# Kernel tuning notes

Hardware: AMD Instinct MI355X
Metric: run time of the kernel (lower is better)

Reference implementation:

```python
import jax, jax.numpy as jnp
import numpy as np

DIM = 64   # model dim == d_inner (expand=1)
Hh = 64
Ww = 64
BATCH = 4
D_IN = 64
N_ST = 8   # d_state
DT_R = 4   # dt_rank = ceil(dim/16)
K = 4      # depthwise conv kernel
NB = 8     # total CrossMambaBlocks: 4 (depth=1) + 4 final cross blocks


def setup_inputs():
    key = jax.random.key(0)
    ks = iter(jax.random.split(key, 40))
    def rn(shape, s=0.02):
        return jax.random.normal(next(ks), shape, jnp.float32) * s
    A_init = jnp.log(jnp.tile(jnp.arange(1, N_ST + 1, dtype=jnp.float32), (NB, D_IN, 1)))
    return dict(
        img1=rn((BATCH, DIM, Hh, Ww), 1.0), img2=rn((BATCH, DIM, Hh, Ww), 1.0),
        img1_sum=rn((BATCH, DIM, Hh, Ww), 1.0), img2_sum=rn((BATCH, DIM, Hh, Ww), 1.0),
        norm0_w=jnp.ones((NB, DIM)), norm0_b=jnp.zeros((NB, DIM)),
        norm1_w=jnp.ones((NB, DIM)), norm1_b=jnp.zeros((NB, DIM)),
        in_w=rn((NB, 2 * D_IN, DIM)), in_b=jnp.zeros((NB, 2 * D_IN)),
        conv_w_f=rn((NB, D_IN, 1, K), 0.1), conv_b_f=jnp.zeros((NB, D_IN)),
        conv_w_b=rn((NB, D_IN, 1, K), 0.1), conv_b_b=jnp.zeros((NB, D_IN)),
        xproj_w_f=rn((NB, DT_R + 2 * N_ST, D_IN)), xproj_w_b=rn((NB, DT_R + 2 * N_ST, D_IN)),
        dtproj_w_f=rn((NB, D_IN, DT_R), 0.1), dtproj_b_f=jnp.zeros((NB, D_IN)),
        dtproj_w_b=rn((NB, D_IN, DT_R), 0.1), dtproj_b_b=jnp.zeros((NB, D_IN)),
        A_log_f=A_init, A_log_b=A_init,
        D_f=jnp.ones((NB, D_IN)), D_b=jnp.ones((NB, D_IN)),
        ln_w=jnp.ones((NB, D_IN)), ln_b=jnp.zeros((NB, D_IN)),
        mout_w=rn((NB, DIM, D_IN)), mout_b=jnp.zeros((NB, DIM)),
        fop_w=rn((DIM, 2 * DIM)), fop_b=jnp.zeros((DIM,)),
    )


def _ln(x, w, b):
    m = x.mean(-1, keepdims=True)
    v = ((x - m) ** 2).mean(-1, keepdims=True)
    return (x - m) * jax.lax.rsqrt(v + 1e-5) * w + b


def _dwconv(x, w, b):
    # x: [b,L,d], w: [d,1,K] depthwise causal conv along L
    y = jax.lax.conv_general_dilated(
        x.transpose(0, 2, 1), w, (1,), [(K - 1, 0)],
        dimension_numbers=('NCH', 'OIH', 'NCH'),
        feature_group_count=x.shape[-1])
    return y.transpose(0, 2, 1) + b


def _ssm(u, dt, Bm, Cm, A, Dm):
    # u,dt: [b,L,d]; Bm,Cm: [b,L,n]; A: [d,n]; Dm: [d]
    dA = jnp.exp(dt[..., None] * A)                 # [b,L,d,n]
    dBu = (dt * u)[..., None] * Bm[:, :, None, :]   # [b,L,d,n]
    def step(h, xs):
        dA_t, dBu_t, C_t = xs
        h = dA_t * h + dBu_t
        return h, jnp.einsum('bdn,bn->bd', h, C_t)
    h0 = jnp.zeros(u.shape[:1] + A.shape, u.dtype)
    _, ys = jax.lax.scan(step, h0, (jnp.moveaxis(dA, 1, 0), jnp.moveaxis(dBu, 1, 0), jnp.moveaxis(Cm, 1, 0)))
    return jnp.moveaxis(ys, 0, 1) + u * Dm


def _direction(x_in, extra, conv_w, conv_b, xproj_w, dtproj_w, dtproj_b, A_log, Dm, flip):
    if flip:
        x_in = x_in[:, ::-1]
        extra = extra[:, ::-1]
    u = jax.nn.silu(_dwconv(x_in, conv_w, conv_b))
    dbl = jnp.einsum('bld,ed->ble', extra, xproj_w)     # cross: dt/B/C from extra embedding
    dtr = dbl[..., :DT_R]
    Bm = dbl[..., DT_R:DT_R + N_ST]
    Cm = dbl[..., DT_R + N_ST:]
    dt = jax.nn.softplus(jnp.einsum('blr,dr->bld', dtr, dtproj_w) + dtproj_b)
    y = _ssm(u, dt, Bm, Cm, -jnp.exp(A_log), Dm)
    if flip:
        y = y[:, ::-1]
    return y


def _cross_block(i, x, extra, p):
    skip = x
    x = _ln(x, p['norm0_w'][i], p['norm0_b'][i])
    extra = _ln(extra, p['norm1_w'][i], p['norm1_b'][i])
    xz = jnp.einsum('bld,ed->ble', x, p['in_w'][i]) + p['in_b'][i]
    x_in, z = xz[..., :D_IN], xz[..., D_IN:]
    y_f = _direction(x_in, extra, p['conv_w_f'][i], p['conv_b_f'][i], p['xproj_w_f'][i],
                     p['dtproj_w_f'][i], p['dtproj_b_f'][i], p['A_log_f'][i], p['D_f'][i], False)
    y_b = _direction(x_in, extra, p['conv_w_b'][i], p['conv_b_b'][i], p['xproj_w_b'][i],
                     p['dtproj_w_b'][i], p['dtproj_b_b'][i], p['A_log_b'][i], p['D_b'][i], True)
    y = 0.5 * (y_f + y_b)                    # if_devide_out=True
    y = _ln(y, p['ln_w'][i], p['ln_b'][i])   # use_norm=True
    y = y * jax.nn.silu(z)
    out = jnp.einsum('bld,ed->ble', y, p['mout_w'][i]) + p['mout_b'][i]
    return out + skip


def _forward(img1, img2, img1_sum, img2_sum, norm0_w, norm0_b, norm1_w, norm1_b, in_w, in_b,
             conv_w_f, conv_b_f, conv_w_b, conv_b_b, xproj_w_f, xproj_w_b,
             dtproj_w_f, dtproj_b_f, dtproj_w_b, dtproj_b_b, A_log_f, A_log_b,
             D_f, D_b, ln_w, ln_b, mout_w, mout_b, fop_w, fop_b):
    p = dict(norm0_w=norm0_w, norm0_b=norm0_b, norm1_w=norm1_w, norm1_b=norm1_b,
             in_w=in_w, in_b=in_b, conv_w_f=conv_w_f, conv_b_f=conv_b_f,
             conv_w_b=conv_w_b, conv_b_b=conv_b_b, xproj_w_f=xproj_w_f, xproj_w_b=xproj_w_b,
             dtproj_w_f=dtproj_w_f, dtproj_b_f=dtproj_b_f, dtproj_w_b=dtproj_w_b,
             dtproj_b_b=dtproj_b_b, A_log_f=A_log_f, A_log_b=A_log_b, D_f=D_f, D_b=D_b,
             ln_w=ln_w, ln_b=ln_b, mout_w=mout_w, mout_b=mout_b)
    def seq(t):
        b, c, h, w = t.shape
        return t.reshape(b, c, h * w).transpose(0, 2, 1)   # b (h w) c
    s1, s2, s1s, s2s = seq(img1), seq(img2), seq(img1_sum), seq(img2_sum)
    # depth=1 cross-fusion loop
    s1 = _cross_block(0, s1, s1s, p)
    s2 = _cross_block(1, s2, s2s, p)
    s1s = _cross_block(2, s1s, s1, p)
    s2s = _cross_block(3, s2s, s2, p)
    # final cross blocks
    i1l = _cross_block(4, s1, s2, p)
    i1g = _cross_block(5, s1, s2s, p)
    i2l = _cross_block(6, s2, s1, p)
    i2g = _cross_block(7, s2, s1s, p)
    c1 = jnp.concatenate([i1l, i1g], -1)
    c2 = jnp.concatenate([i2l, i2g], -1)
    fusion = jnp.einsum('ble,ce->blc', 0.5 * (c1 + c2), fop_w) + fop_b
    b = img1.shape[0]
    return fusion.transpose(0, 2, 1).reshape(b, DIM, Hh, Ww)


def reference(img1, img2, img1_sum, img2_sum, norm0_w, norm0_b, norm1_w, norm1_b, in_w, in_b,
              conv_w_f, conv_b_f, conv_w_b, conv_b_b, xproj_w_f, xproj_w_b,
              dtproj_w_f, dtproj_b_f, dtproj_w_b, dtproj_b_b, A_log_f, A_log_b,
              D_f, D_b, ln_w, ln_b, mout_w, mout_b, fop_w, fop_b):
    return _forward(img1, img2, img1_sum, img2_sum, norm0_w, norm0_b, norm1_w, norm1_b, in_w, in_b,
                    conv_w_f, conv_b_f, conv_w_b, conv_b_b, xproj_w_f, xproj_w_b,
                    dtproj_w_f, dtproj_b_f, dtproj_w_b, dtproj_b_b, A_log_f, A_log_b,
                    D_f, D_b, ln_w, ln_b, mout_w, mout_b, fop_w, fop_b)
```

## Files before the change

### kernel.cpp

```cpp
#include <hip/hip_runtime.h>
#include <hip/hip_bf16.h>

#define BX 4
#define LX 4096
#define DX 64
#define NX 8
#define TCH 16
#define NCH 256
#define BLD (BX*LX*DX)

typedef unsigned short u16;
typedef __attribute__((ext_vector_type(8))) short v8s;
typedef __attribute__((ext_vector_type(4))) float v4f;

#define L2E 1.44269504088896f
#define LN2 0.69314718055994531f

__device__ __forceinline__ float b2f(u16 u){ return __uint_as_float(((unsigned)u)<<16); }
__device__ __forceinline__ u16 f2b(float f){
  unsigned u = __float_as_uint(f);
  unsigned r = (u + 0x7FFFu + ((u>>16)&1u)) >> 16;
  return (u16)r;
}
__device__ __forceinline__ float siluf(float x){
  return x * __builtin_amdgcn_rcpf(1.f + __builtin_amdgcn_exp2f(-x*L2E));
}
__device__ __forceinline__ float softplusf(float x){
  const float t = __builtin_amdgcn_exp2f(-fabsf(x)*L2E);
  return fmaxf(x, 0.f) + LN2 * __builtin_amdgcn_logf(1.f + t);
}

__device__ __forceinline__ v4f mfma16(v8s a, v8s b, v4f c){
  return __builtin_amdgcn_mfma_f32_16x16x32_bf16(a, b, c, 0, 0, 0);
}
__device__ __forceinline__ void split8(const float* v, v8s& hi, v8s& lo){
  #pragma unroll
  for(int j=0;j<8;j++){
    const short h = (short)f2b(v[j]);
    hi[j] = h;
    lo[j] = (short)f2b(v[j] - b2f((u16)h));
  }
}
__device__ __forceinline__ void afrag(const float* tile, int lane, int k0, v8s& hi, v8s& lo){
  const float* p = tile + (lane&15)*72 + k0 + ((lane>>4)<<3);
  float v[8];
  const float4 a = *(const float4*)(p);
  const float4 b = *(const float4*)(p+4);
  v[0]=a.x; v[1]=a.y; v[2]=a.z; v[3]=a.w;
  v[4]=b.x; v[5]=b.y; v[6]=b.z; v[7]=b.w;
  split8(v, hi, lo);
}

struct Ctx {
  const float *nw0,*nb0,*nw1,*nb1;
  const float *inw,*inb;
  const float *convw,*convb;
  const float *xproj;
  const float *dtw,*dtb;
  const float *A2,*Dp;
  const float *lnw,*lnb;
  const float *moutw,*moutb;
  const float *fopw,*fopb;
  const u16 *wih,*wil,*wxh,*wxl,*wmh,*wml,*wfh,*wfl;
  float *act[4], *outc[4];
  float *xin[4], *zz[4], *dbl[4], *yy[4], *Pp[4], *qq[4], *hin[4];
};

struct BlkDesc { int i; const float* x; const float* e; float* out; int slot; };
struct StageArgs { BlkDesc d[4]; };

struct PrepEnt { const void* src; float* dst; int n; int mode; };
struct PrepAll { PrepEnt a[26]; };

__global__ __launch_bounds__(256) void k_prep(PrepAll pa, const u16* df){
  const bool isbf = (df[0] == 0x3F80u);
  PrepEnt p = pa.a[blockIdx.y];
  int idx = blockIdx.x*256 + threadIdx.x;
  if(idx < p.n){
    float v = isbf ? b2f(((const u16*)p.src)[idx]) : ((const float*)p.src)[idx];
    if(p.mode==2) v = -__expf(v) * L2E;
    p.dst[idx] = v;
  }
}

struct WPrep { const float* src; u16* dh; u16* dl; int E; int KS; int kind; int i; };
struct WPrepAll { WPrep a[25]; };

__global__ __launch_bounds__(64) void k_prepw(WPrepAll wa, const float* xprojbase){
  WPrep p = wa.a[blockIdx.y];
  const int NT = (p.E + 15) >> 4;
  const int idx = blockIdx.x;
  if(idx >= NT*p.KS) return;
  const int ct = idx / p.KS, ks = idx % p.KS;
  const int lane = threadIdx.x;
  const int g  = ct*16 + (lane & 15);
  const int k0 = ks*32 + ((lane>>4)<<3);
  const int K  = p.KS*32;
  bool valid; const float* srcp = nullptr;
  if(p.kind == 1){
    valid = (g < 40);
    if(valid){ const int dir = g/20, e = g - dir*20;
      srcp = xprojbase + ((size_t)(dir*8 + p.i)*20 + e)*64 + k0; }
  } else {
    valid = (g < p.E);
    if(valid) srcp = p.src + (size_t)g*K + k0;
  }
  float v[8];
  #pragma unroll
  for(int j=0;j<8;j++) v[j] = valid ? srcp[j] : 0.f;
  v8s hi, lo; split8(v, hi, lo);
  const size_t o = ((size_t)idx*64 + lane)*8;
  *(v8s*)(p.dh + o) = hi;
  *(v8s*)(p.dl + o) = lo;
}

struct SeqArgs { const void* src[4]; };

__global__ __launch_bounds__(256) void k_seq(SeqArgs s, Ctx c, const u16* df){
  const bool isbf = (df[0] == 0x3F80u);
  __shared__ float ld[64*65];
  const int t = blockIdx.z, b = blockIdx.y, l0 = blockIdx.x*64;
  float* dst = c.act[t];
  const int tx = threadIdx.x, ty = threadIdx.y;
  if(isbf){
    const u16* src = (const u16*)s.src[t];
    #pragma unroll
    for(int k=0;k<16;k++){ int d = k*4+ty; ld[d*65+tx] = b2f(src[(size_t)(b*64+d)*LX + l0+tx]); }
  } else {
    const float* src = (const float*)s.src[t];
    #pragma unroll
    for(int k=0;k<16;k++){ int d = k*4+ty; ld[d*65+tx] = src[(size_t)(b*64+d)*LX + l0+tx]; }
  }
  __syncthreads();
  #pragma unroll
  for(int k=0;k<16;k++){ int p = k*4+ty; dst[(size_t)(b*LX + l0+p)*64 + tx] = ld[tx*65+p]; }
}

__device__ __forceinline__ void coop72(float* sb, const float* g, int t){
  #pragma unroll
  for(int k=0;k<4;k++){
    const int idx = k*256 + t;
    const int row = idx >> 4;
    const int c4  = (idx & 15) << 2;
    *(float4*)(sb + row*72 + c4) = *(const float4*)(g + (size_t)row*64 + c4);
  }
}
__device__ __forceinline__ void coop72_avg(float* sb, const float* g0, const float* g1, int t){
  #pragma unroll
  for(int k=0;k<4;k++){
    const int idx = k*256 + t;
    const int row = idx >> 4;
    const int c4  = (idx & 15) << 2;
    const float4 a = *(const float4*)(g0 + (size_t)row*64 + c4);
    const float4 b = *(const float4*)(g1 + (size_t)row*64 + c4);
    float4 o; o.x=0.5f*(a.x+b.x); o.y=0.5f*(a.y+b.y); o.z=0.5f*(a.z+b.z); o.w=0.5f*(a.w+b.w);
    *(float4*)(sb + row*72 + c4) = o;
  }
}

__device__ __forceinline__ void ln72(float* sb, int lane, const float* w, const float* b){
  float r[64];
  float* p = sb + lane*72;
  #pragma unroll
  for(int cc=0;cc<64;cc+=4){ float4 v = *(const float4*)(p+cc); r[cc]=v.x; r[cc+1]=v.y; r[cc+2]=v.z; r[cc+3]=v.w; }
  float m=0.f;
  #pragma unroll
  for(int d=0;d<64;d++) m += r[d];
  m *= (1.f/64.f);
  float va=0.f;
  #pragma unroll
  for(int d=0;d<64;d++){ float t=r[d]-m; va += t*t; }
  va *= (1.f/64.f);
  const float rs = rsqrtf(va + 1e-5f);
  #pragma unroll
  for(int d=0;d<64;d++) r[d] = (r[d]-m)*rs*w[d] + b[d];
  #pragma unroll
  for(int cc=0;cc<64;cc+=4){ float4 v={r[cc],r[cc+1],r[cc+2],r[cc+3]}; *(float4*)(p+cc)=v; }
}

__global__ __launch_bounds__(256) void k_front(Ctx c, StageArgs sa){
  __shared__ __align__(16) float sx[64*72];
  __shared__ __align__(16) float se[64*72];
  const BlkDesc bd = sa.d[blockIdx.y];
  const int i = bd.i;
  const int tile = blockIdx.x;
  const int b = tile >> 6;
  const int l0 = (tile & 63) << 6;
  const int bl0 = b*LX + l0;
  const int t = threadIdx.x;
  const int wave = t >> 6, lane = t & 63;

  coop72(sx, bd.x + (size_t)bl0*64, t);
  coop72(se, bd.e + (size_t)bl0*64, t);
  __syncthreads();
  if(wave == 0)      ln72(sx, lane, c.nw0 + i*64, c.nb0 + i*64);
  else if(wave == 1) ln72(se, lane, c.nw1 + i*64, c.nb1 + i*64);
  __syncthreads();

  const int m0 = wave*16;
  const int q  = lane >> 4;
  const int n15 = lane & 15;

  {
    v8s ah[2], al[2];
    afrag(sx + m0*72, lane, 0,  ah[0], al[0]);
    afrag(sx + m0*72, lane, 32, ah[1], al[1]);
    const v8s* WH = (const v8s*)c.wih + (size_t)i*1024;
    const v8s* WL = (const v8s*)c.wil + (size_t)i*1024;
    #pragma unroll 1
    for(int ct=0; ct<8; ct++){
      const int colg = ct*16 + n15;
      const float bias = c.inb[i*128 + colg];
      v4f acc = {bias, bias, bias, bias};
      #pragma unroll
      for(int ks=0; ks<2; ks++){
        const v8s wh = WH[(ct*2+ks)*64 + lane];
        const v8s wl = WL[(ct*2+ks)*64 + lane];
        acc = mfma16(ah[ks], wl, acc);
        acc = mfma16(al[ks], wh, acc);
        acc = mfma16(ah[ks], wh, acc);
      }
      float* baseo = (colg < 64) ? c.xin[bd.slot] : c.zz[bd.slot];
      const int col = colg & 63;
      #pragma unroll
      for(int r=0;r<4;r++){
        const int row = m0 + q*4 + r;
        baseo[(size_t)(bl0+row)*64 + col] = acc[r];
      }
    }
  }
  {
    v8s ah[2], al[2];
    afrag(se + m0*72, lane, 0,  ah[0], al[0]);
    afrag(se + m0*72, lane, 32, ah[1], al[1]);
    const v8s* WH = (const v8s*)c.wxh + (size_t)i*384;
    const v8s* WL = (const v8s*)c.wxl + (size_t)i*384;
    #pragma unroll 1
    for(int ct=0; ct<3; ct++){
      v4f acc = {0.f,0.f,0.f,0.f};
      #pragma unroll
      for(int ks=0; ks<2; ks++){
        const v8s wh = WH[(ct*2+ks)*64 + lane];
        const v8s wl = WL[(ct*2+ks)*64 + lane];
        acc = mfma16(ah[ks], wl, acc);
        acc = mfma16(al[ks], wh, acc);
        acc = mfma16(ah[ks], wh, acc);
      }
      const int g = ct*16 + n15;
      if(g < 40){
        const int dir = (g >= 20);
        const int e = g - dir*20;
        float* dp = c.dbl[bd.slot] + (size_t)dir*((size_t)BX*LX*20);
        #pragma unroll
        for(int r=0;r<4;r++){
          const int row = m0 + q*4 + r;
          dp[(size_t)(bl0+row)*20 + e] = acc[r];
        }
      }
    }
  }
}

template<int PASS>
__device__ __forceinline__ void scan_body(const Ctx& c, const StageArgs& sa){
  __shared__ float meta[TCH*20];
  const int zid = blockIdx.z;
  const int j = zid >> 1, dir = zid & 1;
  const BlkDesc bd = sa.d[j];
  const int i = bd.i, slot = bd.slot;
  const int ch = blockIdx.x, b = blockIdx.y;
  const int d = threadIdx.x;
  const int pb = (dir*8 + i)*64 + d;

  const float4 cwv = *(const float4*)(c.convw + (size_t)pb*4);
  const float  cbv = c.convb[pb];
  const float4 dwv = *(const float4*)(c.dtw + (size_t)pb*4);
  const float  dtbv = c.dtb[pb];
  const float4 A2a = *(const float4*)(c.A2 + (size_t)pb*8);
  const float4 A2b = *(const float4*)(c.A2 + (size_t)pb*8 + 4);
  float A2[8] = {A2a.x,A2a.y,A2a.z,A2a.w,A2b.x,A2b.y,A2b.z,A2b.w};

  {
    const float4* s = (const float4*)(c.dbl[slot] + (size_t)dir*((size_t)BX*LX*20)
                                      + (size_t)(b*LX + ch*TCH)*20);
    float4* dst = (float4*)meta;
    #pragma unroll
    for(int k=0;k<2;k++){ int idx = k*64 + d; if(idx < 80) dst[idx] = s[idx]; }
  }
  __syncthreads();

  const float* X = c.xin[slot] + (size_t)b*LX*64 + d;
  float h[8];
  if(PASS==1){
    #pragma unroll
    for(int n=0;n<8;n++) h[n]=0.f;
  } else {
    const float* hp = c.hin[slot] + (size_t)(dir*NCH + ch)*((size_t)BX*512) + (size_t)b*512 + d;
    #pragma unroll
    for(int n=0;n<8;n++) h[n] = hp[n*64];
  }
  const float Dv = (PASS==3) ? c.Dp[pb] : 0.f;
  float* Y = (PASS==3) ? (c.yy[slot] + (size_t)(dir*BX + b)*LX*64 + d) : (float*)0;

  int lbase, sgn;
  if(dir==0){ lbase = ch*TCH;          sgn =  1; }
  else      { lbase = ch*TCH + TCH-1;  sgn = -1; }
  float w0,w1,w2;
  { int p0 = lbase - 3*sgn; w0 = (p0>=0 && p0<LX)? X[(size_t)p0*64] : 0.f; }
  { int p1 = lbase - 2*sgn; w1 = (p1>=0 && p1<LX)? X[(size_t)p1*64] : 0.f; }
  { int p2 = lbase - 1*sgn; w2 = (p2>=0 && p2<LX)? X[(size_t)p2*64] : 0.f; }

  const float* Xp = X + (size_t)lbase*64;
  float* Yp = (PASS==3) ? (Y + (size_t)lbase*64) : (float*)0;
  const float* mp = meta + (dir ? (TCH-1)*20 : 0);
  const int xstep = sgn*64;
  const int mstep = sgn*20;

  float S = 0.f;
  #pragma unroll 4
  for(int t=0;t<TCH;t++){
    const float xc = *Xp;
    const float u = siluf(cwv.x*w0 + cwv.y*w1 + cwv.z*w2 + cwv.w*xc + cbv);
    const float4 m0  = *(const float4*)(mp);
    const float4 mb0 = *(const float4*)(mp+4);
    const float4 mb1 = *(const float4*)(mp+8);
    const float dt = softplusf(m0.x*dwv.x + m0.y*dwv.y + m0.z*dwv.z + m0.w*dwv.w + dtbv);
    const float du = dt*u;
    const float Bv[8] = {mb0.x,mb0.y,mb0.z,mb0.w,mb1.x,mb1.y,mb1.z,mb1.w};
    #pragma unroll
    for(int n=0;n<8;n++){
      const float dA = __builtin_amdgcn_exp2f(dt*A2[n]);
      h[n] = dA*h[n] + du*Bv[n];
    }
    if(PASS==3){
      const float4 mc0 = *(const float4*)(mp+12);
      const float4 mc1 = *(const float4*)(mp+16);
      const float Cv[8] = {mc0.x,mc0.y,mc0.z,mc0.w,mc1.x,mc1.y,mc1.z,mc1.w};
      float yv = u*Dv;
      #pragma unroll
      for(int n=0;n<8;n++) yv += h[n]*Cv[n];
      *Yp = yv;
      Yp += xstep;
    } else {
      S += dt;
    }
    w0=w1; w1=w2; w2=xc;
    Xp += xstep; mp += mstep;
  }
  if(PASS==1){
    float* Pw = c.Pp[slot] + (size_t)(dir*NCH + ch)*((size_t)BX*512) + (size_t)b*512 + d;
    float* Qw = c.qq[slot] + (size_t)(dir*NCH + ch)*((size_t)BX*512) + (size_t)b*512 + d;
    #pragma unroll
    for(int n=0;n<8;n++){
      Pw[n*64] = __builtin_amdgcn_exp2f(A2[n]*S);
      Qw[n*64] = h[n];
    }
  }
}

__global__ __launch_bounds__(64) void k_scan1(Ctx c, StageArgs sa){ scan_body<1>(c, sa); }
__global__ __launch_bounds__(64) void k_scan3(Ctx c, StageArgs sa){ scan_body<3>(c, sa); }

__global__ __launch_bounds__(64) void k_mid(Ctx c, StageArgs sa){
  const int b = blockIdx.x >> 3;
  const int seg = blockIdx.x & 7;
  const int dir = blockIdx.y & 1, j = blockIdx.y >> 1;
  const BlkDesc bd = sa.d[j];
  const int slot = bd.slot;
  const int nd = seg*64 + threadIdx.x;
  const size_t base = (size_t)dir*NCH*((size_t)BX*512) + (size_t)b*512 + nd;
  const size_t STR = (size_t)BX*512;
  const float* P = c.Pp[slot] + base;
  const float* Q = c.qq[slot] + base;
  float* H = c.hin[slot] + base;
  float h = 0.f;
  float Pv[16], Qv[16];
  #pragma unroll 1
  for(int g=0; g<NCH/16; g++){
    #pragma unroll
    for(int k=0;k<16;k++){
      const int ch = dir ? (NCH-1 - (g*16+k)) : (g*16+k);
      Pv[k] = P[(size_t)ch*STR]; Qv[k] = Q[(size_t)ch*STR];
    }
    #pragma unroll
    for(int k=0;k<16;k++){
      const int ch = dir ? (NCH-1 - (g*16+k)) : (g*16+k);
      H[(size_t)ch*STR] = h;
      h = fmaf(Pv[k], h, Qv[k]);
    }
  }
}

__global__ __launch_bounds__(256) void k_back(Ctx c, StageArgs sa){
  __shared__ __align__(16) float sy[64*72];
  __shared__ __align__(16) float sz[64*72];
  __shared__ __align__(16) float sk[64*72];
  const BlkDesc bd = sa.d[blockIdx.y];
  const int i = bd.i, slot = bd.slot;
  const int tile = blockIdx.x;
  const int b = tile >> 6;
  const int l0 = (tile & 63) << 6;
  const int bl0 = b*LX + l0;
  const int t = threadIdx.x;
  const int wave = t >> 6, lane = t & 63;

  coop72_avg(sy, c.yy[slot] + (size_t)b*LX*64 + (size_t)l0*64,
                 c.yy[slot] + (size_t)(BX+b)*LX*64 + (size_t)l0*64, t);
  coop72(sz, c.zz[slot] + (size_t)bl0*64, t);
  coop72(sk, bd.x + (size_t)bl0*64, t);
  __syncthreads();
  if(wave == 0){
    ln72(sy, lane, c.lnw + i*64, c.lnb + i*64);
    float* p = sy + lane*72;
    const float* zp = sz + lane*72;
    #pragma unroll
    for(int d=0;d<64;d++){ const float zv = zp[d]; p[d] *= siluf(zv)/(zv==0.f?1.f:zv)*zv; }
  }
  __syncthreads();

  const int m0 = wave*16;
  const int q  = lane >> 4;
  const int n15 = lane & 15;
  v8s ah[2], al[2];
  afrag(sy + m0*72, lane, 0,  ah[0], al[0]);
  afrag(sy + m0*72, lane, 32, ah[1], al[1]);
  const v8s* WH = (const v8s*)c.wmh + (size_t)i*512;
  const v8s* WL = (const v8s*)c.wml + (size_t)i*512;
  #pragma unroll 1
  for(int ct=0; ct<4; ct++){
    const int col = ct*16 + n15;
    const float bias = c.moutb[i*64 + col];
    v4f acc = {bias, bias, bias, bias};
    #pragma unroll
    for(int ks=0; ks<2; ks++){
      const v8s wh = WH[(ct*2+ks)*64 + lane];
      const v8s wl = WL[(ct*2+ks)*64 + lane];
      acc = mfma16(ah[ks], wl, acc);
      acc = mfma16(al[ks], wh, acc);
      acc = mfma16(ah[ks], wh, acc);
    }
    #pragma unroll
    for(int r=0;r<4;r++){
      const int row = m0 + q*4 + r;
      bd.out[(size_t)(bl0+row)*64 + col] = acc[r] + sk[row*72 + col];
    }
  }
}

__global__ __launch_bounds__(256) void k_fusion(Ctx c, void* outp, const u16* df){
  const bool isbf = (df[0] == 0x3F80u);
  __shared__ __align__(16) float sL[64*72];
  __shared__ __align__(16) float sH[64*72];
  __shared__ __align__(16) float sT[64*68];
  const int tile = blockIdx.x;
  const int b = tile >> 6;
  const int l0 = (tile & 63) << 6;
  const int bl0 = b*LX + l0;
  const int t = threadIdx.x;
  const int wave = t >> 6, lane = t & 63;

  coop72_avg(sL, c.outc[0] + (size_t)bl0*64, c.outc[2] + (size_t)bl0*64, t);
  coop72_avg(sH, c.outc[1] + (size_t)bl0*64, c.outc[3] + (size_t)bl0*64, t);
  __syncthreads();

  const int m0 = wave*16;
  const int q  = lane >> 4;
  const int n15 = lane & 15;
  v8s ah[4], al[4];
  afrag(sL + m0*72, lane, 0,  ah[0], al[0]);
  afrag(sL + m0*72, lane, 32, ah[1], al[1]);
  afrag(sH + m0*72, lane, 0,  ah[2], al[2]);
  afrag(sH + m0*72, lane, 32, ah[3], al[3]);
  const v8s* WH = (const v8s*)c.wfh;
  const v8s* WL = (const v8s*)c.wfl;
  #pragma unroll 1
  for(int ct=0; ct<4; ct++){
    const int col = ct*16 + n15;
    const float bias = c.fopb[col];
    v4f acc = {bias, bias, bias, bias};
    #pragma unroll
    for(int ks=0; ks<4; ks++){
      const v8s wh = WH[(ct*4+ks)*64 + lane];
      const v8s wl = WL[(ct*4+ks)*64 + lane];
      acc = mfma16(ah[ks], wl, acc);
      acc = mfma16(al[ks], wh, acc);
      acc = mfma16(ah[ks], wh, acc);
    }
    #pragma unroll
    for(int r=0;r<4;r++) sT[col*68 + m0 + q*4 + r] = acc[r];
  }
  __syncthreads();

  const int o  = t >> 2;
  const int p0 = (t & 3) * 16;
  float v[16];
  #pragma unroll
  for(int k=0;k<16;k+=4){
    const float4 x = *(const float4*)(sT + o*68 + p0 + k);
    v[k]=x.x; v[k+1]=x.y; v[k+2]=x.z; v[k+3]=x.w;
  }
  const size_t off = (size_t)(b*64+o)*LX + l0 + p0;
  if(isbf){
    u16 hb[16];
    #pragma unroll
    for(int k=0;k<16;k++) hb[k] = f2b(v[k]);
    uint4 u0, u1;
    u0.x = hb[0] | ((unsigned)hb[1]<<16);  u0.y = hb[2] | ((unsigned)hb[3]<<16);
    u0.z = hb[4] | ((unsigned)hb[5]<<16);  u0.w = hb[6] | ((unsigned)hb[7]<<16);
    u1.x = hb[8] | ((unsigned)hb[9]<<16);  u1.y = hb[10]| ((unsigned)hb[11]<<16);
    u1.z = hb[12]| ((unsigned)hb[13]<<16); u1.w = hb[14]| ((unsigned)hb[15]<<16);
    *(uint4*)((u16*)outp + off)     = u0;
    *(uint4*)((u16*)outp + off + 8) = u1;
  } else {
    float* fo = (float*)outp + off;
    #pragma unroll
    for(int k=0;k<16;k+=4){ float4 x={v[k],v[k+1],v[k+2],v[k+3]}; *(float4*)(fo+k)=x; }
  }
}

extern "C" void kernel_launch(void* const* d_in, const int* in_sizes, int n_in,
                              void* d_out, int out_size, void* d_ws, size_t ws_size,
                              hipStream_t stream){
  (void)in_sizes; (void)out_size;
  if(n_in < 30) return;
  const u16* df = (const u16*)d_in[22];
  float* w = (float*)d_ws;
  size_t off = 0;
  auto al = [&](size_t n){ float* p = w + off; off += n; return p; };

  Ctx c;
  float* nw0 = al(512);  float* nb0 = al(512);
  float* nw1 = al(512);  float* nb1 = al(512);
  float* inw = al(65536); float* inb = al(1024);
  float* convw = al(4096); float* convb = al(1024);
  float* xproj = al(20480);
  float* dtw = al(4096); float* dtb = al(1024);
  float* A2 = al(8192);  float* Dp = al(1024);
  float* lnw = al(512);  float* lnb = al(512);
  float* moutw = al(32768); float* moutb = al(512);
  float* fopw = al(8192); float* fopb = al(64);
  c.nw0=nw0; c.nb0=nb0; c.nw1=nw1; c.nb1=nb1;
  c.inw=inw; c.inb=inb; c.convw=convw; c.convb=convb;
  c.xproj=xproj; c.dtw=dtw; c.dtb=dtb; c.A2=A2; c.Dp=Dp;
  c.lnw=lnw; c.lnb=lnb; c.moutw=moutw; c.moutb=moutb; c.fopw=fopw; c.fopb=fopb;

  u16* wih = (u16*)al(32768); u16* wil = (u16*)al(32768);
  u16* wxh = (u16*)al(12288); u16* wxl = (u16*)al(12288);
  u16* wmh = (u16*)al(16384); u16* wml = (u16*)al(16384);
  u16* wfh = (u16*)al(4096);  u16* wfl = (u16*)al(4096);
  c.wih=wih; c.wil=wil; c.wxh=wxh; c.wxl=wxl; c.wmh=wmh; c.wml=wml; c.wfh=wfh; c.wfl=wfl;

  for(int k=0;k<4;k++) c.act[k]  = al(BLD);
  for(int k=0;k<4;k++) c.outc[k] = al(BLD);

  const size_t CHW = 2*(size_t)NCH*BX*512;
  const size_t SLOT = (size_t)BLD + BLD + 2*(size_t)BX*LX*20 + 2*(size_t)BLD + 3*CHW;
  const size_t avail = ws_size/4;
  int nslots = 4;
  while(nslots>1 && off + (size_t)nslots*SLOT > avail) nslots >>= 1;
  for(int s=0;s<nslots;s++){
    c.xin[s]=al(BLD); c.zz[s]=al(BLD); c.dbl[s]=al(2*(size_t)BX*LX*20);
    c.yy[s]=al(2*(size_t)BLD);
    c.Pp[s]=al(CHW); c.qq[s]=al(CHW); c.hin[s]=al(CHW);
  }
  for(int s=nslots;s<4;s++){
    c.xin[s]=c.xin[0]; c.zz[s]=c.zz[0]; c.dbl[s]=c.dbl[0]; c.yy[s]=c.yy[0];
    c.Pp[s]=c.Pp[0]; c.qq[s]=c.qq[0]; c.hin[s]=c.hin[0];
  }

  PrepAll pa;
  int kk = 0;
  auto add = [&](int idx, float* dst, int n, int mode){
    pa.a[kk].src=d_in[idx]; pa.a[kk].dst=dst; pa.a[kk].n=n; pa.a[kk].mode=mode; kk++;
  };
  add(4,  nw0, 512, 0); add(5,  nb0, 512, 0);
  add(6,  nw1, 512, 0); add(7,  nb1, 512, 0);
  add(8,  inw, 65536, 0); add(9, inb, 1024, 0);
  add(10, convw, 2048, 0);      add(11, convb, 512, 0);
  add(12, convw+2048, 2048, 0); add(13, convb+512, 512, 0);
  add(14, xproj, 10240, 0);     add(15, xproj+10240, 10240, 0);
  add(16, dtw, 2048, 0);        add(17, dtb, 512, 0);
  add(18, dtw+2048, 2048, 0);   add(19, dtb+512, 512, 0);
  add(20, A2, 4096, 2);         add(21, A2+4096, 4096, 2);
  add(22, Dp, 512, 0);          add(23, Dp+512, 512, 0);
  add(24, lnw, 512, 0);         add(25, lnb, 512, 0);
  add(26, moutw, 32768, 0);     add(27, moutb, 512, 0);
  add(28, fopw, 8192, 0);       add(29, fopb, 64, 0);
  k_prep<<<dim3(256,26),256,0,stream>>>(pa, df);

  WPrepAll wa;
  for(int i=0;i<8;i++) wa.a[i]    = { inw + (size_t)i*8192,  wih + (size_t)i*8192, wil + (size_t)i*8192, 128, 2, 0, i };
  for(int i=0;i<8;i++) wa.a[8+i]  = { nullptr,               wxh + (size_t)i*3072, wxl + (size_t)i*3072,  48, 2, 1, i };
  for(int i=0;i<8;i++) wa.a[16+i] = { moutw + (size_t)i*4096, wmh + (size_t)i*4096, wml + (size_t)i*4096, 64, 2, 0, i };
  wa.a[24] = { fopw, wfh, wfl, 64, 4, 0, 0 };
  k_prepw<<<dim3(16,25),64,0,stream>>>(wa, xproj);

  SeqArgs sq;
  for(int t=0;t<4;t++) sq.src[t] = d_in[t];
  k_seq<<<dim3(64,BX,4), dim3(64,4), 0, stream>>>(sq, c, df);

  BlkDesc SA[2] = {{0, c.act[0], c.act[2], c.act[0], 0},
                   {1, c.act[1], c.act[3], c.act[1], 0}};
  BlkDesc SB[2] = {{2, c.act[2], c.act[0], c.act[2], 0},
                   {3, c.act[3], c.act[1], c.act[3], 0}};
  BlkDesc SC[4] = {{4, c.act[0], c.act[1], c.outc[0], 0},
                   {5, c.act[0], c.act[3], c.outc[1], 0},
                   {6, c.act[1], c.act[0], c.outc[2], 0},
                   {7, c.act[1], c.act[2], c.outc[3], 0}};

  auto run = [&](BlkDesc* ds, int cnt){
    for(int k=0;k<cnt;k+=nslots){
      int n = cnt-k; if(n>nslots) n = nslots;
      StageArgs sa;
      for(int j=0;j<n;j++){ sa.d[j] = ds[k+j]; sa.d[j].slot = j; }
      for(int j=n;j<4;j++) sa.d[j] = sa.d[0];
      k_front<<<dim3(256,n),      256, 0, stream>>>(c, sa);
      k_scan1<<<dim3(NCH,BX,2*n),  64, 0, stream>>>(c, sa);
      k_mid  <<<dim3(BX*8,2*n),    64, 0, stream>>>(c, sa);
      k_scan3<<<dim3(NCH,BX,2*n),  64, 0, stream>>>(c, sa);
      k_back <<<dim3(256,n),      256, 0, stream>>>(c, sa);
    }
  };
  run(SA,2); run(SB,2); run(SC,4);
  k_fusion<<<256,256,0,stream>>>(c, d_out, df);
}
```

Before: 387.1 us.

## Cache conv+SiLU u and softplus dt from scan pass 1 for reuse in pass 3

Pass 1 of the chunked scan now writes the per-timestep u (conv+SiLU output) and dt (softplus) into a new per-slot workspace buffer. Pass 3 reads them back instead of recomputing the conv window, SiLU and dt projection. Both passes are split into direction-templated cores that fully unroll the chunk and prefetch all inputs into registers first. The gating multiply is also simplified to a plain SiLU. The cost is extra global write and read traffic plus a larger workspace, which may reduce the number of slots that fit.

```diff
diff --git a/kernel.cpp b/kernel.cpp
--- a/kernel.cpp
+++ b/kernel.cpp
@@ -63,7 +63,7 @@
   const float *fopw,*fopb;
   const u16 *wih,*wil,*wxh,*wxl,*wmh,*wml,*wfh,*wfl;
   float *act[4], *outc[4];
-  float *xin[4], *zz[4], *dbl[4], *yy[4], *Pp[4], *qq[4], *hin[4];
+  float *xin[4], *zz[4], *dbl[4], *yy[4], *Pp[4], *qq[4], *hin[4], *ud[4];
 };
 
 struct BlkDesc { int i; const float* x; const float* e; float* out; int slot; };
@@ -261,9 +261,66 @@
   }
 }
 
+template<int SGN>
+__device__ __forceinline__ void scan1_core(const float* Xb, const float* mb, float2* UDb,
+    const float4 cwv, const float cbv, const float4 dwv, const float dtbv,
+    const float* A2, float* h, float& S, float w0, float w1, float w2){
+  float xs[TCH];
+  #pragma unroll
+  for(int t=0;t<TCH;t++) xs[t] = Xb[SGN*t*64];
+  #pragma unroll
+  for(int t=0;t<TCH;t++){
+    const float xc = xs[t];
+    const float u = siluf(cwv.x*w0 + cwv.y*w1 + cwv.z*w2 + cwv.w*xc + cbv);
+    const float* m = mb + SGN*t*20;
+    const float4 m0 = *(const float4*)(m);
+    const float dt = softplusf(m0.x*dwv.x + m0.y*dwv.y + m0.z*dwv.z + m0.w*dwv.w + dtbv);
+    float2 udv; udv.x = u; udv.y = dt;
+    UDb[SGN*t*64] = udv;
+    const float du = dt*u;
+    const float4 mb0 = *(const float4*)(m+4);
+    const float4 mb1 = *(const float4*)(m+8);
+    const float Bv[8] = {mb0.x,mb0.y,mb0.z,mb0.w,mb1.x,mb1.y,mb1.z,mb1.w};
+    #pragma unroll
+    for(int n=0;n<8;n++){
+      const float dA = __builtin_amdgcn_exp2f(dt*A2[n]);
+      h[n] = dA*h[n] + du*Bv[n];
+    }
+    S += dt;
+    w0=w1; w1=w2; w2=xc;
+  }
+}
+template<int SGN>
+__device__ __forceinline__ void scan3_core(const float2* UDb, const float* mb, float* Yb,
+    const float* A2, float* h, const float Dv){
+  float2 ud[TCH];
+  #pragma unroll
+  for(int t=0;t<TCH;t++) ud[t] = UDb[SGN*t*64];
+  #pragma unroll
+  for(int t=0;t<TCH;t++){
+    const float u = ud[t].x, dt = ud[t].y;
+    const float du = dt*u;
+    const float* m = mb + SGN*t*20;
+    const float4 mb0 = *(const float4*)(m+4);
+    const float4 mb1 = *(const float4*)(m+8);
+    const float4 mc0 = *(const float4*)(m+12);
+    const float4 mc1 = *(const float4*)(m+16);
+    const float Bv[8] = {mb0.x,mb0.y,mb0.z,mb0.w,mb1.x,mb1.y,mb1.z,mb1.w};
+    const float Cv[8] = {mc0.x,mc0.y,mc0.z,mc0.w,mc1.x,mc1.y,mc1.z,mc1.w};
+    float yv = u*Dv;
+    #pragma unroll
+    for(int n=0;n<8;n++){
+      const float dA = __builtin_amdgcn_exp2f(dt*A2[n]);
+      h[n] = dA*h[n] + du*Bv[n];
+      yv += h[n]*Cv[n];
+    }
+    Yb[SGN*t*64] = yv;
+  }
+}
+
 template<int PASS>
 __device__ __forceinline__ void scan_body(const Ctx& c, const StageArgs& sa){
-  __shared__ float meta[TCH*20];
+  __shared__ __align__(16) float meta[TCH*20];
   const int zid = blockIdx.z;
   const int j = zid >> 1, dir = zid & 1;
   const BlkDesc bd = sa.d[j];
@@ -272,8 +329,6 @@
   const int d = threadIdx.x;
   const int pb = (dir*8 + i)*64 + d;
 
-  const float4 cwv = *(const float4*)(c.convw + (size_t)pb*4);
-  const float  cbv = c.convb[pb];
   const float4 dwv = *(const float4*)(c.dtw + (size_t)pb*4);
   const float  dtbv = c.dtb[pb];
   const float4 A2a = *(const float4*)(c.A2 + (size_t)pb*8);
@@ -289,7 +344,6 @@
   }
   __syncthreads();
 
-  const float* X = c.xin[slot] + (size_t)b*LX*64 + d;
   float h[8];
   if(PASS==1){
     #pragma unroll
@@ -299,55 +353,24 @@
     #pragma unroll
     for(int n=0;n<8;n++) h[n] = hp[n*64];
   }
-  const float Dv = (PASS==3) ? c.Dp[pb] : 0.f;
-  float* Y = (PASS==3) ? (c.yy[slot] + (size_t)(dir*BX + b)*LX*64 + d) : (float*)0;
-
-  int lbase, sgn;
-  if(dir==0){ lbase = ch*TCH;          sgn =  1; }
-  else      { lbase = ch*TCH + TCH-1;  sgn = -1; }
-  float w0,w1,w2;
-  { int p0 = lbase - 3*sgn; w0 = (p0>=0 && p0<LX)? X[(size_t)p0*64] : 0.f; }
-  { int p1 = lbase - 2*sgn; w1 = (p1>=0 && p1<LX)? X[(size_t)p1*64] : 0.f; }
-  { int p2 = lbase - 1*sgn; w2 = (p2>=0 && p2<LX)? X[(size_t)p2*64] : 0.f; }
-
-  const float* Xp = X + (size_t)lbase*64;
-  float* Yp = (PASS==3) ? (Y + (size_t)lbase*64) : (float*)0;
-  const float* mp = meta + (dir ? (TCH-1)*20 : 0);
-  const int xstep = sgn*64;
-  const int mstep = sgn*20;
-
-  float S = 0.f;
-  #pragma unroll 4
-  for(int t=0;t<TCH;t++){
-    const float xc = *Xp;
-    const float u = siluf(cwv.x*w0 + cwv.y*w1 + cwv.z*w2 + cwv.w*xc + cbv);
-    const float4 m0  = *(const float4*)(mp);
-    const float4 mb0 = *(const float4*)(mp+4);
-    const float4 mb1 = *(const float4*)(mp+8);
-    const float dt = softplusf(m0.x*dwv.x + m0.y*dwv.y + m0.z*dwv.z + m0.w*dwv.w + dtbv);
-    const float du = dt*u;
-    const float Bv[8] = {mb0.x,mb0.y,mb0.z,mb0.w,mb1.x,mb1.y,mb1.z,mb1.w};
-    #pragma unroll
-    for(int n=0;n<8;n++){
-      const float dA = __builtin_amdgcn_exp2f(dt*A2[n]);
-      h[n] = dA*h[n] + du*Bv[n];
-    }
-    if(PASS==3){
-      const float4 mc0 = *(const float4*)(mp+12);
-      const float4 mc1 = *(const float4*)(mp+16);
-      const float Cv[8] = {mc0.x,mc0.y,mc0.z,mc0.w,mc1.x,mc1.y,mc1.z,mc1.w};
-      float yv = u*Dv;
-      #pragma unroll
-      for(int n=0;n<8;n++) yv += h[n]*Cv[n];
-      *Yp = yv;
-      Yp += xstep;
-    } else {
-      S += dt;
-    }
-    w0=w1; w1=w2; w2=xc;
-    Xp += xstep; mp += mstep;
-  }
+
+  const int lbase = dir ? (ch*TCH + TCH-1) : (ch*TCH);
+  float2* UDb = (float2*)c.ud[slot] + ((size_t)(dir*BX + b)*LX + lbase)*64 + d;
+  const float* mb = meta + (dir ? (TCH-1)*20 : 0);
+
   if(PASS==1){
+    const float4 cwv = *(const float4*)(c.convw + (size_t)pb*4);
+    const float  cbv = c.convb[pb];
+    const float* X = c.xin[slot] + (size_t)b*LX*64 + d;
+    float w0,w1,w2;
+    const int sgn = dir ? -1 : 1;
+    { int p0 = lbase - 3*sgn; w0 = (p0>=0 && p0<LX)? X[(size_t)p0*64] : 0.f; }
+    { int p1 = lbase - 2*sgn; w1 = (p1>=0 && p1<LX)? X[(size_t)p1*64] : 0.f; }
+    { int p2 = lbase - 1*sgn; w2 = (p2>=0 && p2<LX)? X[(size_t)p2*64] : 0.f; }
+    const float* Xb = X + (size_t)lbase*64;
+    float S = 0.f;
+    if(dir==0) scan1_core< 1>(Xb, mb, UDb, cwv, cbv, dwv, dtbv, A2, h, S, w0, w1, w2);
+    else       scan1_core<-1>(Xb, mb, UDb, cwv, cbv, dwv, dtbv, A2, h, S, w0, w1, w2);
     float* Pw = c.Pp[slot] + (size_t)(dir*NCH + ch)*((size_t)BX*512) + (size_t)b*512 + d;
     float* Qw = c.qq[slot] + (size_t)(dir*NCH + ch)*((size_t)BX*512) + (size_t)b*512 + d;
     #pragma unroll
@@ -355,6 +378,11 @@
       Pw[n*64] = __builtin_amdgcn_exp2f(A2[n]*S);
       Qw[n*64] = h[n];
     }
+  } else {
+    const float Dv = c.Dp[pb];
+    float* Yb = c.yy[slot] + (size_t)(dir*BX + b)*LX*64 + (size_t)lbase*64 + d;
+    if(dir==0) scan3_core< 1>(UDb, mb, Yb, A2, h, Dv);
+    else       scan3_core<-1>(UDb, mb, Yb, A2, h, Dv);
   }
 }
 
@@ -414,7 +442,7 @@
     float* p = sy + lane*72;
     const float* zp = sz + lane*72;
     #pragma unroll
-    for(int d=0;d<64;d++){ const float zv = zp[d]; p[d] *= siluf(zv)/(zv==0.f?1.f:zv)*zv; }
+    for(int d=0;d<64;d++){ p[d] *= siluf(zp[d]); }
   }
   __syncthreads();
 
@@ -554,7 +582,8 @@
   for(int k=0;k<4;k++) c.outc[k] = al(BLD);
 
   const size_t CHW = 2*(size_t)NCH*BX*512;
-  const size_t SLOT = (size_t)BLD + BLD + 2*(size_t)BX*LX*20 + 2*(size_t)BLD + 3*CHW;
+  const size_t UDW = 2*(size_t)BX*LX*64*2;
+  const size_t SLOT = (size_t)BLD + BLD + 2*(size_t)BX*LX*20 + 2*(size_t)BLD + 3*CHW + UDW;
   const size_t avail = ws_size/4;
   int nslots = 4;
   while(nslots>1 && off + (size_t)nslots*SLOT > avail) nslots >>= 1;
@@ -562,10 +591,11 @@
     c.xin[s]=al(BLD); c.zz[s]=al(BLD); c.dbl[s]=al(2*(size_t)BX*LX*20);
     c.yy[s]=al(2*(size_t)BLD);
     c.Pp[s]=al(CHW); c.qq[s]=al(CHW); c.hin[s]=al(CHW);
+    c.ud[s]=al(UDW);
   }
   for(int s=nslots;s<4;s++){
     c.xin[s]=c.xin[0]; c.zz[s]=c.zz[0]; c.dbl[s]=c.dbl[0]; c.yy[s]=c.yy[0];
-    c.Pp[s]=c.Pp[0]; c.qq[s]=c.qq[0]; c.hin[s]=c.hin[0];
+    c.Pp[s]=c.Pp[0]; c.qq[s]=c.qq[0]; c.hin[s]=c.hin[0]; c.ud[s]=c.ud[0];
   }
 
   PrepAll pa;
```

Measured after the change: 400.0 us. 1.03x slower.
